# Performance work log

Hardware: AMD Instinct MI355X
Metric: run time of the kernel (lower is better)

Reference implementation:

```python
import jax, jax.numpy as jnp
import numpy as np

EMBEDDING_DIM = 100
M = 50                      # chunk width
NUM_CHUNK = EMBEDDING_DIM // M  # 2
VOCAB = 100000
EPS = 1e-8                  # torch CosineSimilarity eps


def setup_inputs() -> dict:
    key = jax.random.key(0)
    k_idx, k_emb, k_w, k_u = jax.random.split(key, 4)
    word_idxs = jax.random.randint(k_idx, (4096, 200), 0, VOCAB)  # [B, L]
    # embedding table initialized uniform(-1, 1) as in the original np.random.uniform
    emb_table = jax.random.uniform(k_emb, (VOCAB, EMBEDDING_DIM), dtype=jnp.float32,
                                   minval=-1.0, maxval=1.0)
    weights = jnp.ones((EMBEDDING_DIM, 1), dtype=jnp.float32)      # output projection
    attend_u = jnp.ones((NUM_CHUNK, M), dtype=jnp.float32)         # per-chunk attention query
    return {"word_idxs": word_idxs, "emb_table": emb_table,
            "weights": weights, "attend_u": attend_u}


def reference(word_idxs, emb_table, weights, attend_u):
    B, L = word_idxs.shape
    embeds = emb_table[word_idxs]                       # [B, L, 100]
    ch = embeds.reshape(B, L, NUM_CHUNK, M)             # [B, L, C, M]
    # cosine similarity per word vs per-chunk query (torch eps semantics)
    e_norm = ch / jnp.maximum(jnp.linalg.norm(ch, axis=-1, keepdims=True), EPS)
    u_norm = attend_u / jnp.maximum(jnp.linalg.norm(attend_u, axis=-1, keepdims=True), EPS)
    cos = jnp.einsum('blcm,cm->blc', e_norm, u_norm)    # [B, L, C]
    alphas = jnp.exp(cos)                               # positive -> L1 norm == sum
    norm_alphas = alphas / jnp.sum(alphas, axis=1, keepdims=True)
    hidden = jnp.einsum('blcm,blc->bcm', ch, norm_alphas).reshape(B, EMBEDDING_DIM)
    return hidden @ weights                             # [B, 1]
```

## Files before the change

### kernel.cpp

```cpp
#include <hip/hip_runtime.h>

constexpr int C_ = 2;
constexpr int M_ = 50;
constexpr int ED = 100;
constexpr float EPS = 1e-8f;

__global__ __launch_bounds__(256, 4) void row_stats_kernel(
    const float* __restrict__ emb,
    const float* __restrict__ wgt,
    const float* __restrict__ att,
    float4*      __restrict__ tbl,
    int vocab)
{
    __shared__ float2 s_uw[ED];
    __shared__ float  s_su[C_];

    const int t = threadIdx.x;
    if (t < ED) s_uw[t] = make_float2(att[t], wgt[t]);
    __syncthreads();
    if (t < C_) {
        float ss = 0.f;
        #pragma unroll
        for (int m = 0; m < M_; ++m) { float v = s_uw[t * M_ + m].x; ss += v * v; }
        s_su[t] = 1.0f / fmaxf(sqrtf(ss), EPS);
    }
    __syncthreads();

    const int r = blockIdx.x * 256 + t;
    if (r >= vocab) return;

    const float4* p = reinterpret_cast<const float4*>(emb + (long long)r * ED);
    float sq0 = 0.f, sq1 = 0.f, du0 = 0.f, du1 = 0.f, dw0 = 0.f, dw1 = 0.f;
    #pragma unroll
    for (int i = 0; i < ED / 4; ++i) {
        const float4 v = p[i];
        const float xs[4] = {v.x, v.y, v.z, v.w};
        #pragma unroll
        for (int k = 0; k < 4; ++k) {
            const int e = 4 * i + k;
            const float x = xs[k];
            const float2 uw = s_uw[e];
            if (e < M_) { sq0 += x * x; du0 = fmaf(x, uw.x, du0); dw0 = fmaf(x, uw.y, dw0); }
            else        { sq1 += x * x; du1 = fmaf(x, uw.x, du1); dw1 = fmaf(x, uw.y, dw1); }
        }
    }
    const float c0 = du0 / fmaxf(sqrtf(sq0), EPS) * s_su[0];
    const float c1 = du1 / fmaxf(sqrtf(sq1), EPS) * s_su[1];
    const float a0 = __expf(c0);
    const float a1 = __expf(c1);
    tbl[r] = make_float4(a0, a1, a0 * dw0, a1 * dw1);
}

__global__ __launch_bounds__(256, 4) void attend_kernel(
    const int*    __restrict__ idx,
    const float4* __restrict__ tbl,
    float*        __restrict__ out,
    int L)
{
    __shared__ float s_red[4][4];
    const int t = threadIdx.x;
    const int b = blockIdx.x;

    float a0 = 0.f, a1 = 0.f, ap0 = 0.f, ap1 = 0.f;
    if (t < L) {
        const int r = idx[(long long)b * L + t];
        const float4 v = tbl[r];
        a0 = v.x; a1 = v.y; ap0 = v.z; ap1 = v.w;
    }

    #pragma unroll
    for (int off = 32; off > 0; off >>= 1) {
        a0  += __shfl_down(a0,  off, 64);
        a1  += __shfl_down(a1,  off, 64);
        ap0 += __shfl_down(ap0, off, 64);
        ap1 += __shfl_down(ap1, off, 64);
    }
    const int wave = t >> 6;
    if ((t & 63) == 0) {
        s_red[wave][0] = a0;  s_red[wave][1] = a1;
        s_red[wave][2] = ap0; s_red[wave][3] = ap1;
    }
    __syncthreads();
    if (t == 0) {
        float A0 = 0.f, A1 = 0.f, P0 = 0.f, P1 = 0.f;
        #pragma unroll
        for (int wv = 0; wv < 4; ++wv) {
            A0 += s_red[wv][0]; A1 += s_red[wv][1];
            P0 += s_red[wv][2]; P1 += s_red[wv][3];
        }
        out[b] = P0 / A0 + P1 / A1;
    }
}

extern "C" void kernel_launch(void* const* d_in, const int* in_sizes, int n_in,
                              void* d_out, int out_size, void* d_ws, size_t ws_size,
                              hipStream_t stream) {
    const int*   idx = (const int*)d_in[0];
    const float* emb = (const float*)d_in[1];
    const float* wgt = (const float*)d_in[2];
    const float* att = (const float*)d_in[3];
    float* out = (float*)d_out;

    const int B     = out_size;
    const int L     = in_sizes[0] / B;
    const int vocab = in_sizes[1] / ED;

    float4* tbl = (float4*)d_ws;

    row_stats_kernel<<<(vocab + 255) / 256, 256, 0, stream>>>(emb, wgt, att, tbl, vocab);
    attend_kernel<<<B, 256, 0, stream>>>(idx, tbl, out, L);
}
```

Baseline: 102.1 us.

## Stage embedding rows through LDS with coalesced loads; one wave per batch row

The row-stats kernel now has each block cooperatively load 128 embedding rows into padded shared memory with coalesced float4 reads. Each thread then computes its row statistics from LDS, which replaces the old strided per-thread row loads. The attend kernel assigns one wavefront per batch row, looping over L with a lane stride, and drops the shared-memory cross-wave reduction and block sync. The cost is roughly 51KB of LDS per block, which limits occupancy, plus scalar LDS stores.

After: 103.2 us. About the same (+1.2%).

```diff
diff --git a/kernel.cpp b/kernel.cpp
--- a/kernel.cpp
+++ b/kernel.cpp
@@ -5,17 +5,23 @@
 constexpr int ED = 100;
 constexpr float EPS = 1e-8f;
 
-__global__ __launch_bounds__(256, 4) void row_stats_kernel(
+constexpr int ROWS = 128;
+constexpr int PAD  = 101;
+
+__global__ __launch_bounds__(128) void row_stats_kernel(
     const float* __restrict__ emb,
     const float* __restrict__ wgt,
     const float* __restrict__ att,
     float4*      __restrict__ tbl,
     int vocab)
 {
+    __shared__ float  s_rows[ROWS * PAD];
     __shared__ float2 s_uw[ED];
     __shared__ float  s_su[C_];
 
-    const int t = threadIdx.x;
+    const int t  = threadIdx.x;
+    const int r0 = blockIdx.x * ROWS;
+
     if (t < ED) s_uw[t] = make_float2(att[t], wgt[t]);
     __syncthreads();
     if (t < C_) {
@@ -24,48 +30,60 @@
         for (int m = 0; m < M_; ++m) { float v = s_uw[t * M_ + m].x; ss += v * v; }
         s_su[t] = 1.0f / fmaxf(sqrtf(ss), EPS);
     }
+
+    const int nrows = min(ROWS, vocab - r0);
+    const int nvec  = nrows * (ED / 4);
+    const float4* src = reinterpret_cast<const float4*>(emb + (long long)r0 * ED);
+    for (int i = t; i < nvec; i += 128) {
+        const float4 v = src[i];
+        const int F   = i * 4;
+        const int row = F / ED;
+        const int col = F - row * ED;
+        float* d = &s_rows[row * PAD + col];
+        d[0] = v.x; d[1] = v.y; d[2] = v.z; d[3] = v.w;
+    }
     __syncthreads();
 
-    const int r = blockIdx.x * 256 + t;
-    if (r >= vocab) return;
-
-    const float4* p = reinterpret_cast<const float4*>(emb + (long long)r * ED);
-    float sq0 = 0.f, sq1 = 0.f, du0 = 0.f, du1 = 0.f, dw0 = 0.f, dw1 = 0.f;
-    #pragma unroll
-    for (int i = 0; i < ED / 4; ++i) {
-        const float4 v = p[i];
-        const float xs[4] = {v.x, v.y, v.z, v.w};
+    if (t < nrows) {
+        const float* row = &s_rows[t * PAD];
+        float sq0 = 0.f, sq1 = 0.f, du0 = 0.f, du1 = 0.f, dw0 = 0.f, dw1 = 0.f;
         #pragma unroll
-        for (int k = 0; k < 4; ++k) {
-            const int e = 4 * i + k;
-            const float x = xs[k];
+        for (int e = 0; e < M_; ++e) {
+            const float x = row[e];
             const float2 uw = s_uw[e];
-            if (e < M_) { sq0 += x * x; du0 = fmaf(x, uw.x, du0); dw0 = fmaf(x, uw.y, dw0); }
-            else        { sq1 += x * x; du1 = fmaf(x, uw.x, du1); dw1 = fmaf(x, uw.y, dw1); }
+            sq0 += x * x; du0 = fmaf(x, uw.x, du0); dw0 = fmaf(x, uw.y, dw0);
         }
+        #pragma unroll
+        for (int e = M_; e < ED; ++e) {
+            const float x = row[e];
+            const float2 uw = s_uw[e];
+            sq1 += x * x; du1 = fmaf(x, uw.x, du1); dw1 = fmaf(x, uw.y, dw1);
+        }
+        const float c0 = du0 / fmaxf(sqrtf(sq0), EPS) * s_su[0];
+        const float c1 = du1 / fmaxf(sqrtf(sq1), EPS) * s_su[1];
+        const float a0 = __expf(c0);
+        const float a1 = __expf(c1);
+        tbl[r0 + t] = make_float4(a0, a1, a0 * dw0, a1 * dw1);
     }
-    const float c0 = du0 / fmaxf(sqrtf(sq0), EPS) * s_su[0];
-    const float c1 = du1 / fmaxf(sqrtf(sq1), EPS) * s_su[1];
-    const float a0 = __expf(c0);
-    const float a1 = __expf(c1);
-    tbl[r] = make_float4(a0, a1, a0 * dw0, a1 * dw1);
 }
 
-__global__ __launch_bounds__(256, 4) void attend_kernel(
+__global__ __launch_bounds__(256) void attend_kernel(
     const int*    __restrict__ idx,
     const float4* __restrict__ tbl,
     float*        __restrict__ out,
-    int L)
+    int B, int L)
 {
-    __shared__ float s_red[4][4];
-    const int t = threadIdx.x;
-    const int b = blockIdx.x;
+    const int wave = threadIdx.x >> 6;
+    const int lane = threadIdx.x & 63;
+    const int b    = blockIdx.x * 4 + wave;
+    if (b >= B) return;
 
+    const int* ib = idx + (long long)b * L;
     float a0 = 0.f, a1 = 0.f, ap0 = 0.f, ap1 = 0.f;
-    if (t < L) {
-        const int r = idx[(long long)b * L + t];
-        const float4 v = tbl[r];
-        a0 = v.x; a1 = v.y; ap0 = v.z; ap1 = v.w;
+    #pragma unroll 4
+    for (int l = lane; l < L; l += 64) {
+        const float4 v = tbl[ib[l]];
+        a0 += v.x; a1 += v.y; ap0 += v.z; ap1 += v.w;
     }
 
     #pragma unroll
@@ -75,21 +93,7 @@
         ap0 += __shfl_down(ap0, off, 64);
         ap1 += __shfl_down(ap1, off, 64);
     }
-    const int wave = t >> 6;
-    if ((t & 63) == 0) {
-        s_red[wave][0] = a0;  s_red[wave][1] = a1;
-        s_red[wave][2] = ap0; s_red[wave][3] = ap1;
-    }
-    __syncthreads();
-    if (t == 0) {
-        float A0 = 0.f, A1 = 0.f, P0 = 0.f, P1 = 0.f;
-        #pragma unroll
-        for (int wv = 0; wv < 4; ++wv) {
-            A0 += s_red[wv][0]; A1 += s_red[wv][1];
-            P0 += s_red[wv][2]; P1 += s_red[wv][3];
-        }
-        out[b] = P0 / A0 + P1 / A1;
-    }
+    if (lane == 0) out[b] = ap0 / a0 + ap1 / a1;
 }
 
 extern "C" void kernel_launch(void* const* d_in, const int* in_sizes, int n_in,
@@ -107,6 +111,6 @@
 
     float4* tbl = (float4*)d_ws;
 
-    row_stats_kernel<<<(vocab + 255) / 256, 256, 0, stream>>>(emb, wgt, att, tbl, vocab);
-    attend_kernel<<<B, 256, 0, stream>>>(idx, tbl, out, L);
+    row_stats_kernel<<<(vocab + ROWS - 1) / ROWS, 128, 0, stream>>>(emb, wgt, att, tbl, vocab);
+    attend_kernel<<<(B + 3) / 4, 256, 0, stream>>>(idx, tbl, out, B, L);
 }
```
